# Kernel tuning notes

Measured on AMD Instinct MI355X. Metric: run time of the kernel, lower is better.

## Reference

```python
import jax, jax.numpy as jnp
import numpy as np

B, S, D = 4, 1024, 1024
H = 16
DH = D // H  # head dim = 64
SCALE = DH ** -0.5
NEG = -1e18


def setup_inputs() -> dict:
    key = jax.random.key(0)
    ks = jax.random.split(key, 8)
    queries = jax.random.normal(ks[0], (B, S, D), dtype=jnp.float32)
    keys_ = jax.random.normal(ks[1], (B, S, D), dtype=jnp.float32)
    values = jax.random.normal(ks[2], (B, S, D), dtype=jnp.float32)
    mask = jax.random.randint(ks[3], (B, 1, S), 0, 2).astype(bool)
    sd = 1.0 / np.sqrt(D)
    Wq = jax.random.normal(ks[4], (D, D), dtype=jnp.float32) * sd
    Wk = jax.random.normal(ks[5], (D, D), dtype=jnp.float32) * sd
    Wv = jax.random.normal(ks[6], (D, D), dtype=jnp.float32) * sd
    Wo = jax.random.normal(ks[7], (D, D), dtype=jnp.float32) * sd
    return {"queries": queries, "keys": keys_, "values": values,
            "Wq": Wq, "Wk": Wk, "Wv": Wv, "Wo": Wo, "mask": mask}


def _split_heads(x):
    # [B,S,D] -> [B,H,S,DH]
    b, s, d = x.shape
    return x.reshape(b, s, H, d // H).transpose(0, 2, 1, 3)


def reference(queries, keys, values, Wq, Wk, Wv, Wo, mask):
    q = _split_heads(queries @ Wq) * SCALE          # [B,H,S,DH]
    k = _split_heads(keys @ Wk)                     # [B,H,S,DH]
    v = _split_heads(values @ Wv)                   # [B,H,S,DH]
    logits = jnp.einsum('bhqd,bhkd->bhqk', q, k)    # [B,H,S,S]
    # mask [B,1,Lk] -> unsqueeze head dim -> broadcast over [B,H,Lq,Lk]
    logits = jnp.where(mask[:, None, :, :], NEG, logits)
    attention_weights = logits.sum(axis=1) / H      # [B,S,S] head-averaged logits
    w = jax.nn.softmax(logits, axis=-1)             # dropout p=0 -> identity
    ctx = jnp.einsum('bhqk,bhkd->bhqd', w, v)       # [B,H,S,DH]
    ctx = ctx.transpose(0, 2, 1, 3).reshape(q.shape[0], q.shape[2], H * DH)
    outputs = ctx @ Wo                              # [B,S,D]
    return (outputs, attention_weights)
```

## Files before the change

### kernel.cpp

```cpp
#include <hip/hip_runtime.h>
#include <hip/hip_bf16.h>

typedef __bf16 bf16;
typedef __attribute__((ext_vector_type(8))) __bf16 bf16x8;
typedef __attribute__((ext_vector_type(4))) __bf16 bf16x4;
typedef __attribute__((ext_vector_type(4))) float f32x4;

#define NEGV (-1e18f)
#define LOG2E 1.4426950408889634f

__device__ __forceinline__ bf16 f2b(float f) {
    unsigned u = __builtin_bit_cast(unsigned, f);
    u += 0x7fffu + ((u >> 16) & 1u);
    unsigned short h = (unsigned short)(u >> 16);
    return __builtin_bit_cast(bf16, h);
}

__device__ __forceinline__ f32x4 mfma16(bf16x8 a, bf16x8 b, f32x4 c) {
    return __builtin_amdgcn_mfma_f32_16x16x32_bf16(a, b, c, 0, 0, 0);
}

__device__ __forceinline__ void gl16(const void* g, void* l) {
    __builtin_amdgcn_global_load_lds((const __attribute__((address_space(1))) void*)g,
                                     (__attribute__((address_space(3))) void*)l, 16, 0, 0);
}

__global__ __launch_bounds__(256) void prep(const float* __restrict__ Qf,
                                            const float* __restrict__ Kf,
                                            const float* __restrict__ Vf,
                                            const float* __restrict__ W0,
                                            const float* __restrict__ W1,
                                            const float* __restrict__ W2,
                                            const float* __restrict__ W3,
                                            bf16* __restrict__ Qa,
                                            bf16* __restrict__ Ka,
                                            bf16* __restrict__ Va,
                                            bf16* __restrict__ Wout) {
    __shared__ float tile[64][65];
    int bx = blockIdx.x;
    int t = threadIdx.x;
    if (bx < 6144) {
        int z = bx >> 11, x = bx & 2047;
        const float* in = (z == 0) ? Qf : (z == 1) ? Kf : Vf;
        bf16* out = (z == 0) ? Qa : (z == 1) ? Ka : Va;
        size_t i = ((size_t)x * 256 + t) * 8;
        float4 a = *(const float4*)&in[i];
        float4 b = *(const float4*)&in[i + 4];
        bf16x8 o;
        o[0] = f2b(a.x); o[1] = f2b(a.y); o[2] = f2b(a.z); o[3] = f2b(a.w);
        o[4] = f2b(b.x); o[5] = f2b(b.y); o[6] = f2b(b.z); o[7] = f2b(b.w);
        *(bf16x8*)&out[i] = o;
        return;
    }
    int w = bx - 6144;
    int z = w >> 8;
    const float* Ws[4] = {W0, W1, W2, W3};
    const float* W = Ws[z];
    bf16* O = Wout + ((size_t)z << 20);
    int k0 = (w & 15) * 64, n0 = ((w >> 4) & 15) * 64;
#pragma unroll
    for (int p = 0; p < 4; p++) {
        int r = (t >> 4) + p * 16, c = (t & 15) * 4;
        float4 v = *(const float4*)&W[(size_t)(k0 + r) * 1024 + n0 + c];
        tile[r][c] = v.x; tile[r][c + 1] = v.y; tile[r][c + 2] = v.z; tile[r][c + 3] = v.w;
    }
    __syncthreads();
#pragma unroll
    for (int p = 0; p < 4; p++) {
        int r = (t >> 4) + p * 16, c = (t & 15) * 4;
        bf16x4 o;
        o[0] = f2b(tile[c][r]); o[1] = f2b(tile[c + 1][r]);
        o[2] = f2b(tile[c + 2][r]); o[3] = f2b(tile[c + 3][r]);
        *(bf16x4*)&O[(size_t)(n0 + r) * 1024 + k0 + c] = o;
    }
}

__global__ __launch_bounds__(256, 3) void gemm_proj3(const bf16* __restrict__ Qa,
                                                     const bf16* __restrict__ Ka,
                                                     const bf16* __restrict__ Va,
                                                     const bf16* __restrict__ WtQ,
                                                     bf16* __restrict__ Qw,
                                                     bf16* __restrict__ Kw,
                                                     bf16* __restrict__ VtG) {
    __shared__ bf16 As[128 * 64];
    __shared__ bf16 Bs[128 * 64];
    char* AsB = (char*)As;
    char* BsB = (char*)Bs;
    int t = threadIdx.x;
    int z = blockIdx.z;
    const bf16* A = (z == 0) ? Qa : (z == 1) ? Ka : Va;
    const bf16* Bt = WtQ + ((size_t)z << 20);
    int m0 = blockIdx.x * 128, n0 = blockIdx.y * 128;
    int wid = t >> 6, lane = t & 63;
    int wr = wid >> 1, wc = wid & 1, lr = lane & 15, lg = lane >> 4;
    f32x4 zero = {0.f, 0.f, 0.f, 0.f};
    f32x4 acc[4][4];
#pragma unroll
    for (int m = 0; m < 4; m++)
#pragma unroll
        for (int n = 0; n < 4; n++) acc[m][n] = zero;

    for (int k0 = 0; k0 < 1024; k0 += 64) {
        __syncthreads();
#pragma unroll
        for (int i = 0; i < 4; i++) {
            int c = wid * 256 + i * 64 + lane;
            int row = c >> 3, q = (c & 7) ^ (row & 7);
            gl16(&A[(size_t)(m0 + row) * 1024 + k0 + q * 8], (void*)&As[c * 8]);
            gl16(&Bt[(size_t)(n0 + row) * 1024 + k0 + q * 8], (void*)&Bs[c * 8]);
        }
        __syncthreads();
#pragma unroll
        for (int kk = 0; kk < 2; kk++) {
            bf16x8 af[4], bfr[4];
#pragma unroll
            for (int m = 0; m < 4; m++) {
                int row = wr * 64 + m * 16 + lr;
                af[m] = *(const bf16x8*)(AsB + ((row * 128 + kk * 64 + lg * 16) ^ ((row & 7) << 4)));
            }
#pragma unroll
            for (int n = 0; n < 4; n++) {
                int row = wc * 64 + n * 16 + lr;
                bfr[n] = *(const bf16x8*)(BsB + ((row * 128 + kk * 64 + lg * 16) ^ ((row & 7) << 4)));
            }
#pragma unroll
            for (int m = 0; m < 4; m++)
#pragma unroll
                for (int n = 0; n < 4; n++) acc[m][n] = mfma16(af[m], bfr[n], acc[m][n]);
        }
    }
#pragma unroll
    for (int n = 0; n < 4; n++) {
        int colg = n0 + wc * 64 + n * 16 + lr;
#pragma unroll
        for (int m = 0; m < 4; m++) {
            int rowg = m0 + wr * 64 + m * 16 + lg * 4;
            if (z == 2) {
                bf16x4 o;
#pragma unroll
                for (int j = 0; j < 4; j++) o[j] = f2b(acc[m][n][j]);
                *(bf16x4*)&VtG[(size_t)colg * 4096 + rowg] = o;
            } else {
                bf16* C = (z == 0) ? Qw : Kw;
                float sc = (z == 0) ? 0.125f : 1.0f;
#pragma unroll
                for (int j = 0; j < 4; j++)
                    C[(size_t)(rowg + j) * 1024 + colg] = f2b(acc[m][n][j] * sc);
            }
        }
    }
}

__global__ __launch_bounds__(256, 3) void gemm_oa(const bf16* __restrict__ CTX,
                                                  const bf16* __restrict__ WtO,
                                                  float* __restrict__ out,
                                                  const bf16* __restrict__ Qw,
                                                  const bf16* __restrict__ Kw,
                                                  float* __restrict__ aw,
                                                  const int* __restrict__ maskp) {
    __shared__ bf16 As[128 * 64];
    __shared__ bf16 Bs[128 * 64];
    char* AsB = (char*)As;
    char* BsB = (char*)Bs;
    int t = threadIdx.x;
    int z = blockIdx.z;
    int bx = blockIdx.x;
    int m0, n0 = blockIdx.y * 128;
    const bf16* A;
    const bf16* Bt;
    float* C;
    const int* mask = nullptr;
    if (z == 0) {
        m0 = bx * 128;
        A = CTX; Bt = WtO; C = out;
    } else {
        int b = bx >> 3;
        m0 = (bx & 7) * 128;
        A = Qw + ((size_t)b << 20); Bt = Kw + ((size_t)b << 20);
        C = aw + ((size_t)b << 20); mask = maskp + b * 1024;
    }
    int wid = t >> 6, lane = t & 63;
    int wr = wid >> 1, wc = wid & 1, lr = lane & 15, lg = lane >> 4;
    f32x4 zero = {0.f, 0.f, 0.f, 0.f};
    f32x4 acc[4][4];
#pragma unroll
    for (int m = 0; m < 4; m++)
#pragma unroll
        for (int n = 0; n < 4; n++) acc[m][n] = zero;

    for (int k0 = 0; k0 < 1024; k0 += 64) {
        __syncthreads();
#pragma unroll
        for (int i = 0; i < 4; i++) {
            int c = wid * 256 + i * 64 + lane;
            int row = c >> 3, q = (c & 7) ^ (row & 7);
            gl16(&A[(size_t)(m0 + row) * 1024 + k0 + q * 8], (void*)&As[c * 8]);
            gl16(&Bt[(size_t)(n0 + row) * 1024 + k0 + q * 8], (void*)&Bs[c * 8]);
        }
        __syncthreads();
#pragma unroll
        for (int kk = 0; kk < 2; kk++) {
            bf16x8 af[4], bfr[4];
#pragma unroll
            for (int m = 0; m < 4; m++) {
                int row = wr * 64 + m * 16 + lr;
                af[m] = *(const bf16x8*)(AsB + ((row * 128 + kk * 64 + lg * 16) ^ ((row & 7) << 4)));
            }
#pragma unroll
            for (int n = 0; n < 4; n++) {
                int row = wc * 64 + n * 16 + lr;
                bfr[n] = *(const bf16x8*)(BsB + ((row * 128 + kk * 64 + lg * 16) ^ ((row & 7) << 4)));
            }
#pragma unroll
            for (int m = 0; m < 4; m++)
#pragma unroll
                for (int n = 0; n < 4; n++) acc[m][n] = mfma16(af[m], bfr[n], acc[m][n]);
        }
    }
#pragma unroll
    for (int n = 0; n < 4; n++) {
        int colg = n0 + wc * 64 + n * 16 + lr;
        int mk = (z == 1) ? mask[colg] : 0;
#pragma unroll
        for (int m = 0; m < 4; m++) {
            int rowg = m0 + wr * 64 + m * 16 + lg * 4;
#pragma unroll
            for (int j = 0; j < 4; j++) {
                float v = acc[m][n][j];
                size_t idx = (size_t)(rowg + j) * 1024 + colg;
                if (z == 0) C[idx] = v;
                else C[idx] = mk ? NEGV : v * (1.f / 16.f);
            }
        }
    }
}

__global__ __launch_bounds__(256, 4) void flash_k(const bf16* __restrict__ Q,
                                                  const bf16* __restrict__ K,
                                                  const bf16* __restrict__ VT,
                                                  bf16* __restrict__ CTX,
                                                  const int* __restrict__ maskp) {
    __shared__ bf16 Ks[2][64 * 64];
    __shared__ bf16 Vs[64 * 64];
    __shared__ bf16 Ps[4][16 * 64];
    __shared__ float biasS[1024];
    int raw = blockIdx.x;
    int idx = raw >> 3;
    int bh = (raw & 7) * 8 + (idx & 7);
    int qt = idx >> 3;
    int b = bh >> 4, h = bh & 15;
    int t = threadIdx.x, wid = t >> 6, lane = t & 63;
    int lr = lane & 15, lg = lane >> 4;
    int qbase = qt * 64 + wid * 16;
    const size_t bS = (size_t)b * 1024;
    char* KsB = (char*)Ks;
    char* VsB = (char*)Vs;
    char* PsW = (char*)&Ps[wid][0];
    const int sxl = (lr & 7) << 4;

    {
        int4 mv = *(const int4*)&maskp[b * 1024 + t * 4];
        float4 bv;
        const float NB = NEGV * LOG2E;
        bv.x = mv.x ? NB : 0.f; bv.y = mv.y ? NB : 0.f;
        bv.z = mv.z ? NB : 0.f; bv.w = mv.w ? NB : 0.f;
        *(float4*)&biasS[t * 4] = bv;
    }

    bf16x8 qf[2];
#pragma unroll
    for (int c = 0; c < 2; c++)
        qf[c] = *(const bf16x8*)&Q[(bS + qbase + lr) * 1024 + h * 64 + c * 32 + lg * 8];

    f32x4 zero = {0.f, 0.f, 0.f, 0.f};
    f32x4 acc[4];
#pragma unroll
    for (int d = 0; d < 4; d++) acc[d] = zero;
    float lsum = 0.f;

    const bf16* Kbase = K + bS * 1024 + h * 64;
    const bf16* Vbase = VT + (size_t)(h * 64) * 4096 + bS;

    int c0 = t, c1 = t + 256;
    int kr0 = c0 >> 3, kq0 = c0 & 7, kr1 = c1 >> 3, kq1 = c1 & 7;
    const int kw0 = (kr0 * 128 + kq0 * 16) ^ ((kr0 & 7) << 4);
    const int kw1 = (kr1 * 128 + kq1 * 16) ^ ((kr1 & 7) << 4);

    {
        bf16x8 t0 = *(const bf16x8*)&Kbase[(size_t)kr0 * 1024 + kq0 * 8];
        bf16x8 t1 = *(const bf16x8*)&Kbase[(size_t)kr1 * 1024 + kq1 * 8];
        *(bf16x8*)(KsB + kw0) = t0;
        *(bf16x8*)(KsB + kw1) = t1;
    }
    bf16x8 kg[2], vg[2];
    vg[0] = *(const bf16x8*)&Vbase[(size_t)kr0 * 4096 + kq0 * 8];
    vg[1] = *(const bf16x8*)&Vbase[(size_t)kr1 * 4096 + kq1 * 8];
    kg[0] = *(const bf16x8*)&Kbase[(size_t)(64 + kr0) * 1024 + kq0 * 8];
    kg[1] = *(const bf16x8*)&Kbase[(size_t)(64 + kr1) * 1024 + kq1 * 8];

    int cur = 0;
    for (int kt = 0; kt < 16; kt++) {
        __syncthreads();
        *(bf16x8*)(VsB + kw0) = vg[0];
        *(bf16x8*)(VsB + kw1) = vg[1];
        if (kt < 15) {
            *(bf16x8*)(KsB + (cur ^ 1) * 8192 + kw0) = kg[0];
            *(bf16x8*)(KsB + (cur ^ 1) * 8192 + kw1) = kg[1];
            size_t ko = (size_t)(kt + 1) * 64;
            vg[0] = *(const bf16x8*)&Vbase[(size_t)kr0 * 4096 + ko + kq0 * 8];
            vg[1] = *(const bf16x8*)&Vbase[(size_t)kr1 * 4096 + ko + kq1 * 8];
            if (kt < 14) {
                kg[0] = *(const bf16x8*)&Kbase[(ko + 64 + kr0) * 1024 + kq0 * 8];
                kg[1] = *(const bf16x8*)&Kbase[(ko + 64 + kr1) * 1024 + kq1 * 8];
            }
        }
        f32x4 s[4];
        __builtin_amdgcn_s_setprio(1);
#pragma unroll
        for (int n = 0; n < 4; n++) {
            int row = n * 16 + lr;
            bf16x8 kf0 = *(const bf16x8*)(KsB + cur * 8192 + ((row * 128 + lg * 16) ^ sxl));
            bf16x8 kf1 = *(const bf16x8*)(KsB + cur * 8192 + ((row * 128 + 64 + lg * 16) ^ sxl));
            f32x4 zz = zero;
            zz = mfma16(kf0, qf[0], zz);
            zz = mfma16(kf1, qf[1], zz);
            s[n] = zz;
        }
        __builtin_amdgcn_s_setprio(0);
        __syncthreads();
        float r0 = 0.f, r1 = 0.f, r2 = 0.f, r3 = 0.f;
#pragma unroll
        for (int n = 0; n < 4; n++) {
            float4 bv = *(const float4*)&biasS[kt * 64 + n * 16 + lg * 4];
            float p0 = __builtin_exp2f(__builtin_fmaf(s[n][0], LOG2E, bv.x));
            float p1 = __builtin_exp2f(__builtin_fmaf(s[n][1], LOG2E, bv.y));
            float p2 = __builtin_exp2f(__builtin_fmaf(s[n][2], LOG2E, bv.z));
            float p3 = __builtin_exp2f(__builtin_fmaf(s[n][3], LOG2E, bv.w));
            r0 += p0; r1 += p1; r2 += p2; r3 += p3;
            bf16x4 o;
            o[0] = (bf16)p0; o[1] = (bf16)p1; o[2] = (bf16)p2; o[3] = (bf16)p3;
            *(bf16x4*)(PsW + ((lr * 128 + n * 32 + lg * 8) ^ sxl)) = o;
        }
        lsum += (r0 + r1) + (r2 + r3);
        __builtin_amdgcn_s_setprio(1);
#pragma unroll
        for (int c = 0; c < 2; c++) {
            bf16x8 pa = *(const bf16x8*)(PsW + ((lr * 128 + c * 64 + lg * 16) ^ sxl));
#pragma unroll
            for (int d = 0; d < 4; d++) {
                int row = d * 16 + lr;
                bf16x8 vb = *(const bf16x8*)(VsB + ((row * 128 + c * 64 + lg * 16) ^ ((row & 7) << 4)));
                acc[d] = mfma16(pa, vb, acc[d]);
            }
        }
        __builtin_amdgcn_s_setprio(0);
        cur ^= 1;
    }
    lsum += __shfl_xor(lsum, 16);
    lsum += __shfl_xor(lsum, 32);
    float lb[4];
#pragma unroll
    for (int j = 0; j < 4; j++) lb[j] = __shfl(lsum, lg * 4 + j);
#pragma unroll
    for (int j = 0; j < 4; j++) {
        float inv = 1.f / lb[j];
#pragma unroll
        for (int d = 0; d < 4; d++)
            CTX[(bS + qbase + lg * 4 + j) * 1024 + h * 64 + d * 16 + lr] = f2b(acc[d][j] * inv);
    }
}

extern "C" void kernel_launch(void* const* d_in, const int* in_sizes, int n_in,
                              void* d_out, int out_size, void* d_ws, size_t ws_size,
                              hipStream_t stream) {
    const float* queries = (const float*)d_in[0];
    const float* keys    = (const float*)d_in[1];
    const float* values  = (const float*)d_in[2];
    const float* Wq = (const float*)d_in[3];
    const float* Wk = (const float*)d_in[4];
    const float* Wv = (const float*)d_in[5];
    const float* Wo = (const float*)d_in[6];
    const int* mask = (const int*)d_in[7];

    float* out = (float*)d_out;
    float* aw  = out + ((size_t)4 << 20);

    bf16* wsb = (bf16*)d_ws;
    bf16* WtQ = wsb;
    bf16* Qa  = wsb + ((size_t)4 << 20);
    bf16* Qw  = wsb + ((size_t)8 << 20);
    bf16* Kw  = wsb + ((size_t)12 << 20);
    bf16* VtG = wsb + ((size_t)16 << 20);
    bf16* Ka  = (bf16*)aw;
    bf16* Va  = (bf16*)aw + ((size_t)4 << 20);
    bf16* CTX = Qa;

    prep<<<dim3(7168), 256, 0, stream>>>(queries, keys, values, Wq, Wk, Wv, Wo,
                                         Qa, Ka, Va, WtQ);
    gemm_proj3<<<dim3(32, 8, 3), 256, 0, stream>>>(Qa, Ka, Va, WtQ, Qw, Kw, VtG);
    flash_k<<<dim3(1024), 256, 0, stream>>>(Qw, Kw, VtG, CTX, mask);
    gemm_oa<<<dim3(32, 8, 2), 256, 0, stream>>>(CTX, WtQ + ((size_t)3 << 20), out,
                                                Qw, Kw, aw, mask);
}
```

Measured before the change: 109.7 us.

## Double-buffer V tiles, drop mid-loop barrier, compute row sums via MFMA

```diff
diff --git a/kernel.cpp b/kernel.cpp
--- a/kernel.cpp
+++ b/kernel.cpp
@@ -235,13 +235,13 @@
     }
 }
 
-__global__ __launch_bounds__(256, 4) void flash_k(const bf16* __restrict__ Q,
+__global__ __launch_bounds__(256, 3) void flash_k(const bf16* __restrict__ Q,
                                                   const bf16* __restrict__ K,
                                                   const bf16* __restrict__ VT,
                                                   bf16* __restrict__ CTX,
                                                   const int* __restrict__ maskp) {
     __shared__ bf16 Ks[2][64 * 64];
-    __shared__ bf16 Vs[64 * 64];
+    __shared__ bf16 Vs[2][64 * 64];
     __shared__ bf16 Ps[4][16 * 64];
     __shared__ float biasS[1024];
     int raw = blockIdx.x;
@@ -272,11 +272,14 @@
     for (int c = 0; c < 2; c++)
         qf[c] = *(const bf16x8*)&Q[(bS + qbase + lr) * 1024 + h * 64 + c * 32 + lg * 8];
 
+    bf16 one1 = __builtin_bit_cast(bf16, (unsigned short)0x3F80);
+    bf16x8 ones = {one1, one1, one1, one1, one1, one1, one1, one1};
+
     f32x4 zero = {0.f, 0.f, 0.f, 0.f};
     f32x4 acc[4];
 #pragma unroll
     for (int d = 0; d < 4; d++) acc[d] = zero;
-    float lsum = 0.f;
+    f32x4 accs = zero;
 
     const bf16* Kbase = K + bS * 1024 + h * 64;
     const bf16* Vbase = VT + (size_t)(h * 64) * 4096 + bS;
@@ -289,29 +292,33 @@
     {
         bf16x8 t0 = *(const bf16x8*)&Kbase[(size_t)kr0 * 1024 + kq0 * 8];
         bf16x8 t1 = *(const bf16x8*)&Kbase[(size_t)kr1 * 1024 + kq1 * 8];
+        bf16x8 u0 = *(const bf16x8*)&Vbase[(size_t)kr0 * 4096 + kq0 * 8];
+        bf16x8 u1 = *(const bf16x8*)&Vbase[(size_t)kr1 * 4096 + kq1 * 8];
         *(bf16x8*)(KsB + kw0) = t0;
         *(bf16x8*)(KsB + kw1) = t1;
+        *(bf16x8*)(VsB + kw0) = u0;
+        *(bf16x8*)(VsB + kw1) = u1;
     }
     bf16x8 kg[2], vg[2];
-    vg[0] = *(const bf16x8*)&Vbase[(size_t)kr0 * 4096 + kq0 * 8];
-    vg[1] = *(const bf16x8*)&Vbase[(size_t)kr1 * 4096 + kq1 * 8];
     kg[0] = *(const bf16x8*)&Kbase[(size_t)(64 + kr0) * 1024 + kq0 * 8];
     kg[1] = *(const bf16x8*)&Kbase[(size_t)(64 + kr1) * 1024 + kq1 * 8];
-
-    int cur = 0;
+    vg[0] = *(const bf16x8*)&Vbase[(size_t)kr0 * 4096 + 64 + kq0 * 8];
+    vg[1] = *(const bf16x8*)&Vbase[(size_t)kr1 * 4096 + 64 + kq1 * 8];
+
     for (int kt = 0; kt < 16; kt++) {
+        int cur = kt & 1;
         __syncthreads();
-        *(bf16x8*)(VsB + kw0) = vg[0];
-        *(bf16x8*)(VsB + kw1) = vg[1];
         if (kt < 15) {
             *(bf16x8*)(KsB + (cur ^ 1) * 8192 + kw0) = kg[0];
             *(bf16x8*)(KsB + (cur ^ 1) * 8192 + kw1) = kg[1];
-            size_t ko = (size_t)(kt + 1) * 64;
-            vg[0] = *(const bf16x8*)&Vbase[(size_t)kr0 * 4096 + ko + kq0 * 8];
-            vg[1] = *(const bf16x8*)&Vbase[(size_t)kr1 * 4096 + ko + kq1 * 8];
+            *(bf16x8*)(VsB + (cur ^ 1) * 8192 + kw0) = vg[0];
+            *(bf16x8*)(VsB + (cur ^ 1) * 8192 + kw1) = vg[1];
             if (kt < 14) {
-                kg[0] = *(const bf16x8*)&Kbase[(ko + 64 + kr0) * 1024 + kq0 * 8];
-                kg[1] = *(const bf16x8*)&Kbase[(ko + 64 + kr1) * 1024 + kq1 * 8];
+                size_t ko = (size_t)(kt + 2) * 64;
+                kg[0] = *(const bf16x8*)&Kbase[(ko + kr0) * 1024 + kq0 * 8];
+                kg[1] = *(const bf16x8*)&Kbase[(ko + kr1) * 1024 + kq1 * 8];
+                vg[0] = *(const bf16x8*)&Vbase[(size_t)kr0 * 4096 + ko + kq0 * 8];
+                vg[1] = *(const bf16x8*)&Vbase[(size_t)kr1 * 4096 + ko + kq1 * 8];
             }
         }
         f32x4 s[4];
@@ -327,8 +334,6 @@
             s[n] = zz;
         }
         __builtin_amdgcn_s_setprio(0);
-        __syncthreads();
-        float r0 = 0.f, r1 = 0.f, r2 = 0.f, r3 = 0.f;
 #pragma unroll
         for (int n = 0; n < 4; n++) {
             float4 bv = *(const float4*)&biasS[kt * 64 + n * 16 + lg * 4];
@@ -336,34 +341,28 @@
             float p1 = __builtin_exp2f(__builtin_fmaf(s[n][1], LOG2E, bv.y));
             float p2 = __builtin_exp2f(__builtin_fmaf(s[n][2], LOG2E, bv.z));
             float p3 = __builtin_exp2f(__builtin_fmaf(s[n][3], LOG2E, bv.w));
-            r0 += p0; r1 += p1; r2 += p2; r3 += p3;
             bf16x4 o;
             o[0] = (bf16)p0; o[1] = (bf16)p1; o[2] = (bf16)p2; o[3] = (bf16)p3;
             *(bf16x4*)(PsW + ((lr * 128 + n * 32 + lg * 8) ^ sxl)) = o;
         }
-        lsum += (r0 + r1) + (r2 + r3);
         __builtin_amdgcn_s_setprio(1);
 #pragma unroll
         for (int c = 0; c < 2; c++) {
             bf16x8 pa = *(const bf16x8*)(PsW + ((lr * 128 + c * 64 + lg * 16) ^ sxl));
+            accs = mfma16(pa, ones, accs);
 #pragma unroll
             for (int d = 0; d < 4; d++) {
                 int row = d * 16 + lr;
-                bf16x8 vb = *(const bf16x8*)(VsB + ((row * 128 + c * 64 + lg * 16) ^ ((row & 7) << 4)));
+                bf16x8 vb = *(const bf16x8*)(VsB + cur * 8192 +
+                                             ((row * 128 + c * 64 + lg * 16) ^ ((row & 7) << 4)));
                 acc[d] = mfma16(pa, vb, acc[d]);
             }
         }
         __builtin_amdgcn_s_setprio(0);
-        cur ^= 1;
-    }
-    lsum += __shfl_xor(lsum, 16);
-    lsum += __shfl_xor(lsum, 32);
-    float lb[4];
-#pragma unroll
-    for (int j = 0; j < 4; j++) lb[j] = __shfl(lsum, lg * 4 + j);
+    }
 #pragma unroll
     for (int j = 0; j < 4; j++) {
-        float inv = 1.f / lb[j];
+        float inv = 1.f / accs[j];
 #pragma unroll
         for (int d = 0; d < 4; d++)
             CTX[(bS + qbase + lg * 4 + j) * 1024 + h * 64 + d * 16 + lr] = f2b(acc[d][j] * inv);
```

New measurement: 113.8 us. 1.04x slower.
